# Optimization experiments

Hardware: AMD Instinct MI355X
Metric: run time of the kernel (lower is better)

Reference implementation:

```python
import jax, jax.numpy as jnp
import numpy as np

N_HEAD = 16
D_HEAD = 64


def setup_inputs() -> dict:
    key = jax.random.key(0)
    k1, k2, k3 = jax.random.split(key, 3)
    B, L, D = 2, 2048, 1024
    inp = jax.random.normal(k1, (B, L, D), dtype=jnp.float32)
    # causal mask: True -> masked (matches torch masked_fill_ semantics)
    mask = jnp.triu(jnp.ones((L, L), dtype=bool), k=1)[None, None, :, :]
    W_qkv = jax.random.normal(k2, (D, 3 * N_HEAD * D_HEAD), dtype=jnp.float32) * 0.02
    b_qkv = jnp.zeros((3 * N_HEAD * D_HEAD,), dtype=jnp.float32)
    W_out = jax.random.normal(k3, (N_HEAD * D_HEAD, D), dtype=jnp.float32) * 0.02
    b_out = jnp.zeros((D,), dtype=jnp.float32)
    return {"input": inp, "mask": mask, "W_qkv": W_qkv, "b_qkv": b_qkv,
            "W_out": W_out, "b_out": b_out}


def reference(input, mask, W_qkv, b_qkv, W_out, b_out):
    B, L, D = input.shape
    qkv = input @ W_qkv + b_qkv                       # [B, L, 3*H*Dh]
    q, k, v = jnp.split(qkv, 3, axis=-1)              # each [B, L, H*Dh]
    qh = q.reshape(B, L, N_HEAD, D_HEAD)
    kh = k.reshape(B, L, N_HEAD, D_HEAD)
    vh = v.reshape(B, L, N_HEAD, D_HEAD)
    scale = 1.0 / (D_HEAD ** 0.5)
    attn = jnp.einsum('bqhd,bkhd->bhqk', qh, kh) * scale  # [B, H, L, L]
    attn = jnp.where(mask, -jnp.inf, attn)
    attn = jax.nn.softmax(attn, axis=-1)
    out = jnp.einsum('bhqk,bkhd->bqhd', attn, vh).reshape(B, L, D)
    out = out @ W_out + b_out
    # next_memory equivalent: (k, v) pre-head-split, as in the torch code
    return (out, k, v)
```

## Files before the change

kernel.cpp:

```cpp
#include <hip/hip_runtime.h>
#include <cstdint>

#define NHEAD 16
#define DHEAD 64
#define SEQ   2048
#define DMODEL 1024
#define MTOT  4096
#define NQKV  3072

typedef __bf16 bf16x8 __attribute__((ext_vector_type(8)));
typedef short  s16x4  __attribute__((ext_vector_type(4)));
typedef float  f32x4  __attribute__((ext_vector_type(4)));

__device__ __forceinline__ unsigned short f2bf(float f) {
  union { float f; unsigned u; } v; v.f = f;
  unsigned r = v.u + 0x7fffu + ((v.u >> 16) & 1u);
  return (unsigned short)(r >> 16);
}

__device__ __forceinline__ void gl_lds16(const void* g, void* l) {
  __builtin_amdgcn_global_load_lds(
      reinterpret_cast<const __attribute__((address_space(1))) unsigned int*>(
          reinterpret_cast<uintptr_t>(g)),
      reinterpret_cast<__attribute__((address_space(3))) unsigned int*>(
          reinterpret_cast<uintptr_t>(l)),
      16, 0, 0);
}

#if __has_builtin(__builtin_amdgcn_mfma_f32_16x16x16bf16_1k)
#define MFMA_PV(a, b, c) __builtin_amdgcn_mfma_f32_16x16x16bf16_1k(a, b, c, 0, 0, 0)
#else
__device__ __forceinline__ f32x4 mfma_pv_asm(s16x4 a, s16x4 b, f32x4 c) {
  f32x4 d;
  asm volatile("v_mfma_f32_16x16x16_bf16 %0, %1, %2, %3"
               : "=v"(d) : "v"(a), "v"(b), "v"(c));
  return d;
}
#define MFMA_PV(a, b, c) mfma_pv_asm(a, b, c)
#endif

__global__ void k_cvt_bf16(const float* __restrict__ x,
                           unsigned short* __restrict__ y, int n4) {
  int i = blockIdx.x * blockDim.x + threadIdx.x;
  if (i >= n4) return;
  float4 v = reinterpret_cast<const float4*>(x)[i];
  ushort4 o;
  o.x = f2bf(v.x); o.y = f2bf(v.y); o.z = f2bf(v.z); o.w = f2bf(v.w);
  reinterpret_cast<ushort4*>(y)[i] = o;
}

__global__ void k_transpose_cvt2(const float* __restrict__ W0, unsigned short* __restrict__ T0,
                                 const float* __restrict__ W1, unsigned short* __restrict__ T1) {
  __shared__ unsigned short t[32][33];
  const int bx = blockIdx.x;
  const float* W = (bx < 96) ? W0 : W1;
  unsigned short* WT = (bx < 96) ? T0 : T1;
  const int N = (bx < 96) ? 3072 : 1024;
  const int n0 = ((bx < 96) ? bx : (bx - 96)) * 32;
  const int k0 = blockIdx.y * 32;
  const int tx = threadIdx.x, ty = threadIdx.y;
  for (int i = ty; i < 32; i += 8)
    t[i][tx] = f2bf(W[(size_t)(k0 + i) * N + n0 + tx]);
  __syncthreads();
  for (int i = ty; i < 32; i += 8)
    WT[(size_t)(n0 + i) * 1024 + k0 + tx] = t[tx][i];
}

__global__ void k_vtrans(const unsigned short* __restrict__ v,
                         unsigned short* __restrict__ vt) {
  __shared__ unsigned short t[32][33];
  const int bh = blockIdx.z;
  const int t0 = blockIdx.x * 32, d0 = blockIdx.y * 32;
  const int tx = threadIdx.x, ty = threadIdx.y;
  const unsigned short* vb = v + (size_t)bh * SEQ * DHEAD;
  unsigned short* vtb = vt + (size_t)bh * DHEAD * SEQ;
  for (int i = ty; i < 32; i += 8)
    t[i][tx] = vb[(size_t)(t0 + i) * DHEAD + d0 + tx];
  __syncthreads();
  for (int i = ty; i < 32; i += 8)
    vtb[(size_t)(d0 + i) * SEQ + t0 + tx] = t[tx][i];
}

__global__ __launch_bounds__(256, 3) void k_gemm_qkv(
    const unsigned short* __restrict__ A, const unsigned short* __restrict__ Bt,
    const float* __restrict__ bias, float* __restrict__ outbase,
    unsigned short* __restrict__ qbf, unsigned short* __restrict__ kbf,
    unsigned short* __restrict__ vbf) {
  __shared__ __attribute__((aligned(16))) unsigned short As[2][128 * 32];
  __shared__ __attribute__((aligned(16))) unsigned short Bs[2][128 * 32];
  const int tid = threadIdx.x, lane = tid & 63;
  const int w = tid >> 6, wm = w >> 1, wn = w & 1;
  const int c = lane & 15, q = lane >> 4;
  const int kc = (c & 3) ^ ((c >> 2) & 3);
  const int bm = blockIdx.x * 128, bn = blockIdx.y * 128;
  const int srow = tid >> 2;
  const int skey = (srow & 3) ^ ((srow >> 2) & 3);
  const int scolsw = (((tid & 3) ^ skey) << 3);
  const unsigned short* Ag = A + (size_t)(bm + srow) * DMODEL + scolsw;
  const unsigned short* Bg = Bt + (size_t)(bn + srow) * DMODEL + scolsw;
  f32x4 acc[4][4] = {};

  gl_lds16(Ag, As[0] + tid * 8);
  gl_lds16(Ag + (size_t)64 * DMODEL, As[0] + 2048 + tid * 8);
  gl_lds16(Bg, Bs[0] + tid * 8);
  gl_lds16(Bg + (size_t)64 * DMODEL, Bs[0] + 2048 + tid * 8);

  for (int kt = 0; kt < 32; ++kt) {
    const int cur = kt & 1;
    __syncthreads();
    if (kt < 31) {
      const int k0 = (kt + 1) * 32;
      gl_lds16(Ag + k0, As[cur ^ 1] + tid * 8);
      gl_lds16(Ag + k0 + (size_t)64 * DMODEL, As[cur ^ 1] + 2048 + tid * 8);
      gl_lds16(Bg + k0, Bs[cur ^ 1] + tid * 8);
      gl_lds16(Bg + k0 + (size_t)64 * DMODEL, Bs[cur ^ 1] + 2048 + tid * 8);
    }
    const int ch = (q ^ kc) << 3;
    bf16x8 af[4], bfr[4];
#pragma unroll
    for (int i = 0; i < 4; ++i)
      af[i] = *reinterpret_cast<const bf16x8*>(As[cur] + (wm * 64 + i * 16 + c) * 32 + ch);
#pragma unroll
    for (int j = 0; j < 4; ++j)
      bfr[j] = *reinterpret_cast<const bf16x8*>(Bs[cur] + (wn * 64 + j * 16 + c) * 32 + ch);
#pragma unroll
    for (int i = 0; i < 4; ++i)
#pragma unroll
      for (int j = 0; j < 4; ++j)
        acc[i][j] = __builtin_amdgcn_mfma_f32_16x16x32_bf16(af[i], bfr[j], acc[i][j], 0, 0, 0);
  }

  const int sec = bn >> 10;
#pragma unroll
  for (int j = 0; j < 4; ++j) {
    const int gn = bn + wn * 64 + j * 16 + c;
    const float bv = bias[gn];
    const int cc = gn & 1023, hh = cc >> 6, dd = cc & 63;
#pragma unroll
    for (int i = 0; i < 4; ++i) {
#pragma unroll
      for (int r = 0; r < 4; ++r) {
        const int gm = bm + wm * 64 + i * 16 + q * 4 + r;
        const int bb = gm >> 11, tok = gm & 2047;
        const float val = acc[i][j][r] + bv;
        const size_t hoff = ((size_t)(bb * NHEAD + hh) * SEQ + tok) * DHEAD + dd;
        if (sec == 0) {
          qbf[hoff] = f2bf(val);
        } else if (sec == 1) {
          outbase[(size_t)4194304 + (size_t)gm * DMODEL + cc] = val;
          kbf[hoff] = f2bf(val);
        } else {
          outbase[(size_t)8388608 + (size_t)gm * DMODEL + cc] = val;
          vbf[hoff] = f2bf(val);
        }
      }
    }
  }
}

__global__ __launch_bounds__(256) void k_attn(
    const unsigned short* __restrict__ qbf, const unsigned short* __restrict__ kbf,
    const unsigned short* __restrict__ vtbf, unsigned short* __restrict__ aout) {
  __shared__ __attribute__((aligned(16))) unsigned short Ks[128 * 64];
  __shared__ __attribute__((aligned(16))) unsigned short Vs[64 * 128];

  const int tid = threadIdx.x, lane = tid & 63, w = tid >> 6;
  const int c = lane & 15, q = lane >> 4;
  const int oo = blockIdx.x >> 5, kk = oo & 7, ssl = oo >> 3;
  const int qsub = (ssl == 0) ? (31 - kk) : (ssl == 1) ? kk
                 : (ssl == 2) ? (23 - kk) : (8 + kk);
  const int bh = blockIdx.x & 31;
  const int kmax = qsub >> 1;
  const size_t hoff = (size_t)bh * SEQ * DHEAD;

  const unsigned short* qg = qbf + hoff + (size_t)(qsub * 64 + w * 16 + c) * DHEAD;
  const bf16x8 qb0 = *reinterpret_cast<const bf16x8*>(qg + q * 8);
  const bf16x8 qb1 = *reinterpret_cast<const bf16x8*>(qg + 32 + q * 8);

  f32x4 o[4] = {};
  float mrun = -__builtin_inff(), lrun = 0.f;
  const float sscale = 0.125f * 1.44269504088896340736f;
  const int qloc = (qsub & 1) * 64 + w * 16 + c;
  const int cx = c & 7;

  const int krow = tid >> 3, kswz = (tid & 7) ^ (krow & 7);
  const int vrow = tid >> 4, vswz = (tid & 15) ^ (vrow & 7);
  const unsigned short* kgb = kbf + hoff;
  const unsigned short* vgb = vtbf + (size_t)bh * DHEAD * SEQ;

  for (int kt = 0; kt <= kmax; ++kt) {
    __syncthreads();
    const unsigned short* kg = kgb + (size_t)kt * 128 * DHEAD;
#pragma unroll
    for (int is = 0; is < 4; ++is)
      gl_lds16(kg + (krow + is * 32) * 64 + kswz * 8, Ks + is * 2048 + tid * 8);
    const unsigned short* vg = vgb + kt * 128;
#pragma unroll
    for (int is = 0; is < 4; ++is)
      gl_lds16(vg + (size_t)(vrow + is * 16) * SEQ + vswz * 8, Vs + is * 2048 + tid * 8);
    __syncthreads();

    f32x4 s[8];
#pragma unroll
    for (int mi = 0; mi < 8; ++mi) {
      const unsigned short* kr = Ks + (mi * 16 + c) * 64;
      const bf16x8 ak0 = *reinterpret_cast<const bf16x8*>(kr + (q ^ cx) * 8);
      const bf16x8 ak1 = *reinterpret_cast<const bf16x8*>(kr + ((4 + q) ^ cx) * 8);
      f32x4 t = {};
      t = __builtin_amdgcn_mfma_f32_16x16x32_bf16(ak0, qb0, t, 0, 0, 0);
      t = __builtin_amdgcn_mfma_f32_16x16x32_bf16(ak1, qb1, t, 0, 0, 0);
      s[mi] = t;
    }

    if (kt == kmax) {
#pragma unroll
      for (int mi = 0; mi < 8; ++mi)
#pragma unroll
        for (int r = 0; r < 4; ++r)
          if (mi * 16 + q * 4 + r > qloc) s[mi][r] = -__builtin_inff();
    }

    float mx = -__builtin_inff();
#pragma unroll
    for (int mi = 0; mi < 8; ++mi)
#pragma unroll
      for (int r = 0; r < 4; ++r) mx = fmaxf(mx, s[mi][r]);
    mx = fmaxf(mx, __shfl_xor(mx, 16));
    mx = fmaxf(mx, __shfl_xor(mx, 32));
    const float mn = fmaxf(mrun, mx * sscale);
    const float al = __builtin_amdgcn_exp2f(mrun - mn);
    mrun = mn;

    float rs = 0.f;
    s16x4 pb[8];
#pragma unroll
    for (int mi = 0; mi < 8; ++mi) {
      const float p0 = __builtin_amdgcn_exp2f(__builtin_fmaf(s[mi][0], sscale, -mn));
      const float p1 = __builtin_amdgcn_exp2f(__builtin_fmaf(s[mi][1], sscale, -mn));
      const float p2 = __builtin_amdgcn_exp2f(__builtin_fmaf(s[mi][2], sscale, -mn));
      const float p3 = __builtin_amdgcn_exp2f(__builtin_fmaf(s[mi][3], sscale, -mn));
      rs += (p0 + p1) + (p2 + p3);
      union { s16x4 v; unsigned u[2]; } pk;
      pk.u[0] = __builtin_amdgcn_perm(__float_as_uint(p1), __float_as_uint(p0), 0x07060302u);
      pk.u[1] = __builtin_amdgcn_perm(__float_as_uint(p3), __float_as_uint(p2), 0x07060302u);
      pb[mi] = pk.v;
    }
    rs += __shfl_xor(rs, 16);
    rs += __shfl_xor(rs, 32);
    lrun = lrun * al + rs;
#pragma unroll
    for (int dm = 0; dm < 4; ++dm) o[dm] *= al;

#pragma unroll
    for (int dm = 0; dm < 4; ++dm) {
      const unsigned short* vr = Vs + (dm * 16 + c) * 128 + (q & 1) * 4;
#pragma unroll
      for (int kf = 0; kf < 8; ++kf) {
        const s16x4 av = *reinterpret_cast<const s16x4*>(
            vr + (((kf * 2 + (q >> 1)) ^ cx) * 8));
        o[dm] = MFMA_PV(av, pb[kf], o[dm]);
      }
    }
  }

  const float linv = 1.0f / lrun;
  const int b = bh >> 4, h = bh & 15;
  const int row = b * SEQ + qsub * 64 + w * 16 + c;
#pragma unroll
  for (int dm = 0; dm < 4; ++dm) {
    ushort4 ov;
    ov.x = f2bf(o[dm][0] * linv);
    ov.y = f2bf(o[dm][1] * linv);
    ov.z = f2bf(o[dm][2] * linv);
    ov.w = f2bf(o[dm][3] * linv);
    *reinterpret_cast<ushort4*>(aout + (size_t)row * DMODEL + h * 64 + dm * 16 + q * 4) = ov;
  }
}

__global__ __launch_bounds__(256) void k_gemm_out(
    const unsigned short* __restrict__ A, const unsigned short* __restrict__ Bt,
    const float* __restrict__ bias, float* __restrict__ C) {
  __shared__ __attribute__((aligned(16))) unsigned short As[2][128 * 32];
  __shared__ __attribute__((aligned(16))) unsigned short Bs[2][64 * 32];
  const int tid = threadIdx.x, lane = tid & 63;
  const int w = tid >> 6, wm = w >> 1, wn = w & 1;
  const int c = lane & 15, q = lane >> 4;
  const int kc = (c & 3) ^ ((c >> 2) & 3);
  const int bm = blockIdx.x * 128, bn = blockIdx.y * 64;
  const int srow = tid >> 2;
  const int skey = (srow & 3) ^ ((srow >> 2) & 3);
  const int scolsw = (((tid & 3) ^ skey) << 3);
  const unsigned short* Ag = A + (size_t)(bm + srow) * DMODEL + scolsw;
  const unsigned short* Bg = Bt + (size_t)(bn + srow) * DMODEL + scolsw;
  f32x4 acc[4][2] = {};

  gl_lds16(Ag, As[0] + tid * 8);
  gl_lds16(Ag + (size_t)64 * DMODEL, As[0] + 2048 + tid * 8);
  gl_lds16(Bg, Bs[0] + tid * 8);

  for (int kt = 0; kt < 32; ++kt) {
    const int cur = kt & 1;
    __syncthreads();
    if (kt < 31) {
      const int k0 = (kt + 1) * 32;
      gl_lds16(Ag + k0, As[cur ^ 1] + tid * 8);
      gl_lds16(Ag + k0 + (size_t)64 * DMODEL, As[cur ^ 1] + 2048 + tid * 8);
      gl_lds16(Bg + k0, Bs[cur ^ 1] + tid * 8);
    }
    const int ch = (q ^ kc) << 3;
    bf16x8 af[4], bfr[2];
#pragma unroll
    for (int i = 0; i < 4; ++i)
      af[i] = *reinterpret_cast<const bf16x8*>(As[cur] + (wm * 64 + i * 16 + c) * 32 + ch);
#pragma unroll
    for (int j = 0; j < 2; ++j)
      bfr[j] = *reinterpret_cast<const bf16x8*>(Bs[cur] + (wn * 32 + j * 16 + c) * 32 + ch);
#pragma unroll
    for (int i = 0; i < 4; ++i)
#pragma unroll
      for (int j = 0; j < 2; ++j)
        acc[i][j] = __builtin_amdgcn_mfma_f32_16x16x32_bf16(af[i], bfr[j], acc[i][j], 0, 0, 0);
  }

#pragma unroll
  for (int j = 0; j < 2; ++j) {
    const int gn = bn + wn * 32 + j * 16 + c;
    const float bv = bias[gn];
#pragma unroll
    for (int i = 0; i < 4; ++i)
#pragma unroll
      for (int r = 0; r < 4; ++r) {
        const int gm = bm + wm * 64 + i * 16 + q * 4 + r;
        C[(size_t)gm * DMODEL + gn] = acc[i][j][r] + bv;
      }
  }
}

extern "C" void kernel_launch(void* const* d_in, const int* in_sizes, int n_in,
                              void* d_out, int out_size, void* d_ws, size_t ws_size,
                              hipStream_t stream) {
  (void)in_sizes; (void)n_in; (void)out_size; (void)ws_size;
  const float* input = (const float*)d_in[0];
  const float* W_qkv = (const float*)d_in[2];
  const float* b_qkv = (const float*)d_in[3];
  const float* W_out = (const float*)d_in[4];
  const float* b_out = (const float*)d_in[5];
  float* out = (float*)d_out;

  unsigned char* ws = (unsigned char*)d_ws;
  unsigned short* Abf   = (unsigned short*)(ws + 0);
  unsigned short* VTbf  = (unsigned short*)(ws + 0);
  unsigned short* WqkvT = (unsigned short*)(ws + 8388608);
  unsigned short* WoutT = (unsigned short*)(ws + 14680064);
  unsigned short* Qbf   = (unsigned short*)(ws + 16777216);
  unsigned short* Kbf   = (unsigned short*)(ws + 25165824);
  unsigned short* Vbf   = (unsigned short*)(ws + 33554432);
  unsigned short* Aout  = (unsigned short*)(ws + 41943040);

  k_cvt_bf16<<<4096, 256, 0, stream>>>(input, Abf, 1048576);
  k_transpose_cvt2<<<dim3(128, 32), dim3(32, 8), 0, stream>>>(W_qkv, WqkvT, W_out, WoutT);
  k_gemm_qkv<<<dim3(32, 24), 256, 0, stream>>>(Abf, WqkvT, b_qkv, out, Qbf, Kbf, Vbf);
  k_vtrans<<<dim3(64, 2, 32), dim3(32, 8), 0, stream>>>(Vbf, VTbf);
  k_attn<<<1024, 256, 0, stream>>>(Qbf, Kbf, VTbf, Aout);
  k_gemm_out<<<dim3(32, 16), 256, 0, stream>>>(Aout, WoutT, b_out, out);
}
```

Baseline: 203.8 us.

## Fuse prepass kernels, write V transposed from QKV GEMM, prefetch K in attention

Merges the input conversion and weight transpose kernels into one launch. The QKV GEMM epilogue now writes V directly in transposed layout, which removes the separate V transpose kernel and its round trip through memory. In the attention kernel, the next K tile is prefetched into registers and then stored to LDS, an extra barrier is added before the PV stage, and MFMA sections are wrapped in s_setprio. The extra barrier and register pressure could offset some of the gain.

Result: slower. 212.9 us (+4.5%).

```diff
diff --git a/kernel.cpp b/kernel.cpp
--- a/kernel.cpp
+++ b/kernel.cpp
@@ -39,53 +39,40 @@
 #define MFMA_PV(a, b, c) mfma_pv_asm(a, b, c)
 #endif
 
-__global__ void k_cvt_bf16(const float* __restrict__ x,
-                           unsigned short* __restrict__ y, int n4) {
-  int i = blockIdx.x * blockDim.x + threadIdx.x;
-  if (i >= n4) return;
-  float4 v = reinterpret_cast<const float4*>(x)[i];
-  ushort4 o;
-  o.x = f2bf(v.x); o.y = f2bf(v.y); o.z = f2bf(v.z); o.w = f2bf(v.w);
-  reinterpret_cast<ushort4*>(y)[i] = o;
-}
-
-__global__ void k_transpose_cvt2(const float* __restrict__ W0, unsigned short* __restrict__ T0,
-                                 const float* __restrict__ W1, unsigned short* __restrict__ T1) {
+__global__ void k_prepass(const float* __restrict__ x, unsigned short* __restrict__ y,
+                          const float* __restrict__ W0, unsigned short* __restrict__ T0,
+                          const float* __restrict__ W1, unsigned short* __restrict__ T1) {
   __shared__ unsigned short t[32][33];
-  const int bx = blockIdx.x;
-  const float* W = (bx < 96) ? W0 : W1;
-  unsigned short* WT = (bx < 96) ? T0 : T1;
-  const int N = (bx < 96) ? 3072 : 1024;
-  const int n0 = ((bx < 96) ? bx : (bx - 96)) * 32;
-  const int k0 = blockIdx.y * 32;
-  const int tx = threadIdx.x, ty = threadIdx.y;
-  for (int i = ty; i < 32; i += 8)
-    t[i][tx] = f2bf(W[(size_t)(k0 + i) * N + n0 + tx]);
-  __syncthreads();
-  for (int i = ty; i < 32; i += 8)
-    WT[(size_t)(n0 + i) * 1024 + k0 + tx] = t[tx][i];
-}
-
-__global__ void k_vtrans(const unsigned short* __restrict__ v,
-                         unsigned short* __restrict__ vt) {
-  __shared__ unsigned short t[32][33];
-  const int bh = blockIdx.z;
-  const int t0 = blockIdx.x * 32, d0 = blockIdx.y * 32;
-  const int tx = threadIdx.x, ty = threadIdx.y;
-  const unsigned short* vb = v + (size_t)bh * SEQ * DHEAD;
-  unsigned short* vtb = vt + (size_t)bh * DHEAD * SEQ;
-  for (int i = ty; i < 32; i += 8)
-    t[i][tx] = vb[(size_t)(t0 + i) * DHEAD + d0 + tx];
-  __syncthreads();
-  for (int i = ty; i < 32; i += 8)
-    vtb[(size_t)(d0 + i) * SEQ + t0 + tx] = t[tx][i];
+  const int bid = blockIdx.x;
+  if (bid < 4096) {
+    const int i = bid * 256 + threadIdx.x;
+    float4 v = reinterpret_cast<const float4*>(x)[i];
+    ushort4 o;
+    o.x = f2bf(v.x); o.y = f2bf(v.y); o.z = f2bf(v.z); o.w = f2bf(v.w);
+    reinterpret_cast<ushort4*>(y)[i] = o;
+  } else {
+    const int b2 = bid - 4096;
+    const int bx = b2 & 127;
+    const int by = b2 >> 7;
+    const float* W = (bx < 96) ? W0 : W1;
+    unsigned short* WT = (bx < 96) ? T0 : T1;
+    const int N = (bx < 96) ? 3072 : 1024;
+    const int n0 = ((bx < 96) ? bx : (bx - 96)) * 32;
+    const int k0 = by * 32;
+    const int tx = threadIdx.x & 31, ty = threadIdx.x >> 5;
+    for (int i = ty; i < 32; i += 8)
+      t[i][tx] = f2bf(W[(size_t)(k0 + i) * N + n0 + tx]);
+    __syncthreads();
+    for (int i = ty; i < 32; i += 8)
+      WT[(size_t)(n0 + i) * 1024 + k0 + tx] = t[tx][i];
+  }
 }
 
 __global__ __launch_bounds__(256, 3) void k_gemm_qkv(
     const unsigned short* __restrict__ A, const unsigned short* __restrict__ Bt,
     const float* __restrict__ bias, float* __restrict__ outbase,
     unsigned short* __restrict__ qbf, unsigned short* __restrict__ kbf,
-    unsigned short* __restrict__ vbf) {
+    unsigned short* __restrict__ vtbf) {
   __shared__ __attribute__((aligned(16))) unsigned short As[2][128 * 32];
   __shared__ __attribute__((aligned(16))) unsigned short Bs[2][128 * 32];
   const int tid = threadIdx.x, lane = tid & 63;
@@ -138,21 +125,33 @@
     const int cc = gn & 1023, hh = cc >> 6, dd = cc & 63;
 #pragma unroll
     for (int i = 0; i < 4; ++i) {
-#pragma unroll
-      for (int r = 0; r < 4; ++r) {
-        const int gm = bm + wm * 64 + i * 16 + q * 4 + r;
-        const int bb = gm >> 11, tok = gm & 2047;
-        const float val = acc[i][j][r] + bv;
-        const size_t hoff = ((size_t)(bb * NHEAD + hh) * SEQ + tok) * DHEAD + dd;
-        if (sec == 0) {
-          qbf[hoff] = f2bf(val);
-        } else if (sec == 1) {
-          outbase[(size_t)4194304 + (size_t)gm * DMODEL + cc] = val;
-          kbf[hoff] = f2bf(val);
-        } else {
-          outbase[(size_t)8388608 + (size_t)gm * DMODEL + cc] = val;
-          vbf[hoff] = f2bf(val);
+      const int gm0 = bm + wm * 64 + i * 16 + q * 4;
+      const int bb = gm0 >> 11, tok = gm0 & 2047;
+      if (sec == 0) {
+#pragma unroll
+        for (int r = 0; r < 4; ++r) {
+          const float val = acc[i][j][r] + bv;
+          qbf[((size_t)(bb * NHEAD + hh) * SEQ + tok + r) * DHEAD + dd] = f2bf(val);
         }
+      } else if (sec == 1) {
+#pragma unroll
+        for (int r = 0; r < 4; ++r) {
+          const float val = acc[i][j][r] + bv;
+          outbase[(size_t)4194304 + (size_t)(gm0 + r) * DMODEL + cc] = val;
+          kbf[((size_t)(bb * NHEAD + hh) * SEQ + tok + r) * DHEAD + dd] = f2bf(val);
+        }
+      } else {
+        float vals[4];
+#pragma unroll
+        for (int r = 0; r < 4; ++r) {
+          vals[r] = acc[i][j][r] + bv;
+          outbase[(size_t)8388608 + (size_t)(gm0 + r) * DMODEL + cc] = vals[r];
+        }
+        ushort4 tv;
+        tv.x = f2bf(vals[0]); tv.y = f2bf(vals[1]);
+        tv.z = f2bf(vals[2]); tv.w = f2bf(vals[3]);
+        *reinterpret_cast<ushort4*>(
+            vtbf + ((size_t)(bb * NHEAD + hh) * DHEAD + dd) * SEQ + tok) = tv;
       }
     }
   }
@@ -188,19 +187,31 @@
   const unsigned short* kgb = kbf + hoff;
   const unsigned short* vgb = vtbf + (size_t)bh * DHEAD * SEQ;
 
+  uint4 kreg[4];
+#pragma unroll
+  for (int is = 0; is < 4; ++is)
+    kreg[is] = *reinterpret_cast<const uint4*>(kgb + (krow + is * 32) * 64 + kswz * 8);
+
   for (int kt = 0; kt <= kmax; ++kt) {
     __syncthreads();
-    const unsigned short* kg = kgb + (size_t)kt * 128 * DHEAD;
 #pragma unroll
     for (int is = 0; is < 4; ++is)
-      gl_lds16(kg + (krow + is * 32) * 64 + kswz * 8, Ks + is * 2048 + tid * 8);
+      *reinterpret_cast<uint4*>(Ks + is * 2048 + tid * 8) = kreg[is];
+    __syncthreads();
+
     const unsigned short* vg = vgb + kt * 128;
 #pragma unroll
     for (int is = 0; is < 4; ++is)
       gl_lds16(vg + (size_t)(vrow + is * 16) * SEQ + vswz * 8, Vs + is * 2048 + tid * 8);
-    __syncthreads();
+    if (kt < kmax) {
+      const unsigned short* kg = kgb + (size_t)(kt + 1) * 128 * DHEAD;
+#pragma unroll
+      for (int is = 0; is < 4; ++is)
+        kreg[is] = *reinterpret_cast<const uint4*>(kg + (krow + is * 32) * 64 + kswz * 8);
+    }
 
     f32x4 s[8];
+    __builtin_amdgcn_s_setprio(1);
 #pragma unroll
     for (int mi = 0; mi < 8; ++mi) {
       const unsigned short* kr = Ks + (mi * 16 + c) * 64;
@@ -211,6 +222,7 @@
       t = __builtin_amdgcn_mfma_f32_16x16x32_bf16(ak1, qb1, t, 0, 0, 0);
       s[mi] = t;
     }
+    __builtin_amdgcn_s_setprio(0);
 
     if (kt == kmax) {
 #pragma unroll
@@ -251,6 +263,9 @@
 #pragma unroll
     for (int dm = 0; dm < 4; ++dm) o[dm] *= al;
 
+    __syncthreads();
+
+    __builtin_amdgcn_s_setprio(1);
 #pragma unroll
     for (int dm = 0; dm < 4; ++dm) {
       const unsigned short* vr = Vs + (dm * 16 + c) * 128 + (q & 1) * 4;
@@ -261,6 +276,7 @@
         o[dm] = MFMA_PV(av, pb[kf], o[dm]);
       }
     }
+    __builtin_amdgcn_s_setprio(0);
   }
 
   const float linv = 1.0f / lrun;
@@ -349,18 +365,15 @@
 
   unsigned char* ws = (unsigned char*)d_ws;
   unsigned short* Abf   = (unsigned short*)(ws + 0);
-  unsigned short* VTbf  = (unsigned short*)(ws + 0);
   unsigned short* WqkvT = (unsigned short*)(ws + 8388608);
   unsigned short* WoutT = (unsigned short*)(ws + 14680064);
   unsigned short* Qbf   = (unsigned short*)(ws + 16777216);
   unsigned short* Kbf   = (unsigned short*)(ws + 25165824);
-  unsigned short* Vbf   = (unsigned short*)(ws + 33554432);
+  unsigned short* VTbf  = (unsigned short*)(ws + 33554432);
   unsigned short* Aout  = (unsigned short*)(ws + 41943040);
 
-  k_cvt_bf16<<<4096, 256, 0, stream>>>(input, Abf, 1048576);
-  k_transpose_cvt2<<<dim3(128, 32), dim3(32, 8), 0, stream>>>(W_qkv, WqkvT, W_out, WoutT);
-  k_gemm_qkv<<<dim3(32, 24), 256, 0, stream>>>(Abf, WqkvT, b_qkv, out, Qbf, Kbf, Vbf);
-  k_vtrans<<<dim3(64, 2, 32), dim3(32, 8), 0, stream>>>(Vbf, VTbf);
+  k_prepass<<<8192, 256, 0, stream>>>(input, Abf, W_qkv, WqkvT, W_out, WoutT);
+  k_gemm_qkv<<<dim3(32, 24), 256, 0, stream>>>(Abf, WqkvT, b_qkv, out, Qbf, Kbf, VTbf);
   k_attn<<<1024, 256, 0, stream>>>(Qbf, Kbf, VTbf, Aout);
   k_gemm_out<<<dim3(32, 16), 256, 0, stream>>>(Aout, WoutT, b_out, out);
 }
```

## Merge prepass kernels, add MFMA setprio, stage attention output through LDS

Applied to the files above, without the earlier changes.

Combines the input bf16 conversion and weight transpose into one launch, which removes one kernel launch. It also raises wave priority around the QK and PV MFMA loops in the attention kernel. Finally, the attention output is staged through swizzled LDS so each row is written with coalesced 16-byte stores instead of scattered 8-byte stores. The LDS staging reuses the K buffer after the loop, which is safe only if every wave has finished reading K. That is uncertain without a barrier, although each wave writes only its own slice.

After: 200.7 us. No clear change (-1.5%).

```diff
diff --git a/kernel.cpp b/kernel.cpp
--- a/kernel.cpp
+++ b/kernel.cpp
@@ -39,31 +39,33 @@
 #define MFMA_PV(a, b, c) mfma_pv_asm(a, b, c)
 #endif
 
-__global__ void k_cvt_bf16(const float* __restrict__ x,
-                           unsigned short* __restrict__ y, int n4) {
-  int i = blockIdx.x * blockDim.x + threadIdx.x;
-  if (i >= n4) return;
-  float4 v = reinterpret_cast<const float4*>(x)[i];
-  ushort4 o;
-  o.x = f2bf(v.x); o.y = f2bf(v.y); o.z = f2bf(v.z); o.w = f2bf(v.w);
-  reinterpret_cast<ushort4*>(y)[i] = o;
-}
-
-__global__ void k_transpose_cvt2(const float* __restrict__ W0, unsigned short* __restrict__ T0,
-                                 const float* __restrict__ W1, unsigned short* __restrict__ T1) {
+__global__ void k_prepass(const float* __restrict__ x, unsigned short* __restrict__ y,
+                          const float* __restrict__ W0, unsigned short* __restrict__ T0,
+                          const float* __restrict__ W1, unsigned short* __restrict__ T1) {
   __shared__ unsigned short t[32][33];
-  const int bx = blockIdx.x;
-  const float* W = (bx < 96) ? W0 : W1;
-  unsigned short* WT = (bx < 96) ? T0 : T1;
-  const int N = (bx < 96) ? 3072 : 1024;
-  const int n0 = ((bx < 96) ? bx : (bx - 96)) * 32;
-  const int k0 = blockIdx.y * 32;
-  const int tx = threadIdx.x, ty = threadIdx.y;
-  for (int i = ty; i < 32; i += 8)
-    t[i][tx] = f2bf(W[(size_t)(k0 + i) * N + n0 + tx]);
-  __syncthreads();
-  for (int i = ty; i < 32; i += 8)
-    WT[(size_t)(n0 + i) * 1024 + k0 + tx] = t[tx][i];
+  const int bid = blockIdx.x;
+  if (bid < 4096) {
+    const int i = bid * 256 + threadIdx.x;
+    float4 v = reinterpret_cast<const float4*>(x)[i];
+    ushort4 o;
+    o.x = f2bf(v.x); o.y = f2bf(v.y); o.z = f2bf(v.z); o.w = f2bf(v.w);
+    reinterpret_cast<ushort4*>(y)[i] = o;
+  } else {
+    const int b2 = bid - 4096;
+    const int bx = b2 & 127;
+    const int by = b2 >> 7;
+    const float* W = (bx < 96) ? W0 : W1;
+    unsigned short* WT = (bx < 96) ? T0 : T1;
+    const int N = (bx < 96) ? 3072 : 1024;
+    const int n0 = ((bx < 96) ? bx : (bx - 96)) * 32;
+    const int k0 = by * 32;
+    const int tx = threadIdx.x & 31, ty = threadIdx.x >> 5;
+    for (int i = ty; i < 32; i += 8)
+      t[i][tx] = f2bf(W[(size_t)(k0 + i) * N + n0 + tx]);
+    __syncthreads();
+    for (int i = ty; i < 32; i += 8)
+      WT[(size_t)(n0 + i) * 1024 + k0 + tx] = t[tx][i];
+  }
 }
 
 __global__ void k_vtrans(const unsigned short* __restrict__ v,
@@ -201,6 +203,7 @@
     __syncthreads();
 
     f32x4 s[8];
+    __builtin_amdgcn_s_setprio(1);
 #pragma unroll
     for (int mi = 0; mi < 8; ++mi) {
       const unsigned short* kr = Ks + (mi * 16 + c) * 64;
@@ -211,6 +214,7 @@
       t = __builtin_amdgcn_mfma_f32_16x16x32_bf16(ak1, qb1, t, 0, 0, 0);
       s[mi] = t;
     }
+    __builtin_amdgcn_s_setprio(0);
 
     if (kt == kmax) {
 #pragma unroll
@@ -251,6 +255,7 @@
 #pragma unroll
     for (int dm = 0; dm < 4; ++dm) o[dm] *= al;
 
+    __builtin_amdgcn_s_setprio(1);
 #pragma unroll
     for (int dm = 0; dm < 4; ++dm) {
       const unsigned short* vr = Vs + (dm * 16 + c) * 128 + (q & 1) * 4;
@@ -261,11 +266,11 @@
         o[dm] = MFMA_PV(av, pb[kf], o[dm]);
       }
     }
+    __builtin_amdgcn_s_setprio(0);
   }
 
   const float linv = 1.0f / lrun;
-  const int b = bh >> 4, h = bh & 15;
-  const int row = b * SEQ + qsub * 64 + w * 16 + c;
+  unsigned short* Ws = Ks + w * 1024;
 #pragma unroll
   for (int dm = 0; dm < 4; ++dm) {
     ushort4 ov;
@@ -273,7 +278,18 @@
     ov.y = f2bf(o[dm][1] * linv);
     ov.z = f2bf(o[dm][2] * linv);
     ov.w = f2bf(o[dm][3] * linv);
-    *reinterpret_cast<ushort4*>(aout + (size_t)row * DMODEL + h * 64 + dm * 16 + q * 4) = ov;
+    const int bofs = c * 128 + ((dm * 32 + q * 8) ^ ((c & 7) << 4));
+    *reinterpret_cast<ushort4*>(Ws + (bofs >> 1)) = ov;
+  }
+  const int b = bh >> 4, h = bh & 15;
+#pragma unroll
+  for (int it = 0; it < 2; ++it) {
+    const int r_ = (lane >> 3) + it * 8;
+    const int g = lane & 7;
+    const uint4 val = *reinterpret_cast<const uint4*>(
+        Ws + ((r_ * 128 + (((unsigned)g ^ (r_ & 7)) << 4)) >> 1));
+    const int row = b * SEQ + qsub * 64 + w * 16 + r_;
+    *reinterpret_cast<uint4*>(aout + (size_t)row * DMODEL + h * 64 + g * 8) = val;
   }
 }
 
@@ -357,8 +373,7 @@
   unsigned short* Vbf   = (unsigned short*)(ws + 33554432);
   unsigned short* Aout  = (unsigned short*)(ws + 41943040);
 
-  k_cvt_bf16<<<4096, 256, 0, stream>>>(input, Abf, 1048576);
-  k_transpose_cvt2<<<dim3(128, 32), dim3(32, 8), 0, stream>>>(W_qkv, WqkvT, W_out, WoutT);
+  k_prepass<<<8192, 256, 0, stream>>>(input, Abf, W_qkv, WqkvT, W_out, WoutT);
   k_gemm_qkv<<<dim3(32, 24), 256, 0, stream>>>(Abf, WqkvT, b_qkv, out, Qbf, Kbf, Vbf);
   k_vtrans<<<dim3(64, 2, 32), dim3(32, 8), 0, stream>>>(Vbf, VTbf);
   k_attn<<<1024, 256, 0, stream>>>(Qbf, Kbf, VTbf, Aout);
```
